# Optimization experiments

Measured on AMD Instinct MI355X. Metric: run time of the kernel, lower is better.

The kernel has to match this reference:

```python
import jax, jax.numpy as jnp
import numpy as np
import math

B, L, D, H, MAX_K = 8, 4096, 2048, 16, 1024
HD = D // H


def setup_inputs() -> dict:
    key = jax.random.key(0)
    ks = jax.random.split(key, 20)
    x = jax.random.normal(ks[0], (B, L, D), dtype=jnp.float32)
    register = jax.random.normal(ks[1], (B, D), dtype=jnp.float32)
    # mask with exactly MAX_K True per row -> max_k == MAX_K, no ragged padding
    perms = jax.vmap(lambda k: jax.random.permutation(k, L))(jax.random.split(ks[2], B))
    sel = perms[:, :MAX_K]
    mask = jnp.zeros((B, L), dtype=bool).at[jnp.arange(B)[:, None], sel].set(True)
    s = 1.0 / math.sqrt(D)
    def lin(k):
        k1, k2 = jax.random.split(k)
        return (jax.random.uniform(k1, (D, D), jnp.float32, -s, s),
                jax.random.uniform(k2, (D,), jnp.float32, -s, s))
    Wq, bq = lin(ks[3]); Wk, bk = lin(ks[4]); Wv, bv = lin(ks[5])
    Wrk, brk = lin(ks[6]); Wrv, brv = lin(ks[7]); Wo, bo = lin(ks[8])
    return {"x": x, "mask": mask, "register": register,
            "Wq": Wq, "bq": bq, "Wk": Wk, "bk": bk, "Wv": Wv, "bv": bv,
            "Wrk": Wrk, "brk": brk, "Wrv": Wrv, "brv": brv, "Wo": Wo, "bo": bo}


def reference(x, mask, register, Wq, bq, Wk, bk, Wv, bv, Wrk, brk, Wrv, brv, Wo, bo):
    Bb, Ll, Dd = x.shape
    scale = math.sqrt(HD)
    # stable argsort puts True(=selected) tokens first, in ascending position order
    idx = jnp.argsort(jnp.logical_not(mask), axis=1, stable=True)[:, :MAX_K]  # [B,K]
    pos = idx
    sig = jnp.take_along_axis(x, idx[:, :, None], axis=1)  # [B,K,D]
    Q = (sig @ Wq.T + bq).reshape(Bb, MAX_K, H, HD)
    Kt = (sig @ Wk.T + bk)
    Vt = (sig @ Wv.T + bv)
    Kr = (register @ Wrk.T + brk)[:, None, :]  # [B,1,D]
    Vr = (register @ Wrv.T + brv)[:, None, :]
    Kall = jnp.concatenate([Kt, Kr], axis=1).reshape(Bb, MAX_K + 1, H, HD)
    Vall = jnp.concatenate([Vt, Vr], axis=1).reshape(Bb, MAX_K + 1, H, HD)
    scores = jnp.einsum('bqhd,bkhd->bhqk', Q, Kall) / scale  # [B,H,K,K+1]
    causal = jnp.where(pos[:, :, None] < pos[:, None, :], -1e9, 0.0)  # [B,K,K]
    full_mask = jnp.concatenate([causal, jnp.zeros((Bb, MAX_K, 1), x.dtype)], axis=2)[:, None]
    attn = jax.nn.softmax(scores + full_mask, axis=-1)
    out = jnp.einsum('bhqk,bkhd->bqhd', attn, Vall).reshape(Bb, MAX_K, Dd)
    y = out @ Wo.T + bo
    res = x.at[jnp.arange(Bb)[:, None], idx].set(y)
    return res
```

## Files before the change

### kernel.cpp

```cpp
#include <hip/hip_runtime.h>
#include <hip/hip_bf16.h>

#define B_  8
#define L_  4096
#define D_  2048
#define H_  16
#define HD_ 128
#define MK_ 1024
#define VTP 1040

typedef __attribute__((ext_vector_type(8))) short short8;
typedef __attribute__((ext_vector_type(4))) float f32x4;

__device__ inline unsigned short f2bf(float f) {
  unsigned int u = __float_as_uint(f);
  unsigned int r = (u + 0x7fffu + ((u >> 16) & 1u)) >> 16;
  return (unsigned short)r;
}

__device__ __forceinline__ void gload_lds16(const void* g, void* l) {
  __builtin_amdgcn_global_load_lds(
      (const __attribute__((address_space(1))) void*)g,
      (__attribute__((address_space(3))) void*)l, 16, 0, 0);
}

__global__ void detect_mask_kernel(const unsigned char* __restrict__ mask, int* flag,
                                   unsigned char* __restrict__ sel) {
  __shared__ int cnt;
  if (threadIdx.x == 0) cnt = 0;
  __syncthreads();
  for (int i = threadIdx.x; i < (B_ * L_) / 16; i += 256) ((int4*)sel)[i] = make_int4(0, 0, 0, 0);
  int local = 0;
  for (int i = threadIdx.x; i < B_ * L_; i += 256) local += (mask[i] != 0);
  atomicAdd(&cnt, local);
  __syncthreads();
  if (threadIdx.x == 0) {
    int t = 0;
    if (cnt == B_ * MK_)      t = 0;
    else if (cnt == 2 * MK_)  t = 1;
    else if (cnt == 4 * MK_)  t = 2;
    *flag = t;
  }
}

__global__ void build_rowmap_kernel(const void* __restrict__ maskv,
                                    const int* __restrict__ flag,
                                    int* __restrict__ rowmap,
                                    unsigned char* __restrict__ sel) {
  int b = blockIdx.x;
  int tid = threadIdx.x;
  int t = *flag;
  __shared__ int cnts[256];
  unsigned char loc[16];
  int c = 0;
  for (int j = 0; j < 16; ++j) {
    int pos = tid * 16 + j;
    int mv;
    if (t == 1)      mv = ((const int*)maskv)[b * L_ + pos] != 0;
    else if (t == 2) mv = ((const float*)maskv)[b * L_ + pos] != 0.0f;
    else             mv = ((const unsigned char*)maskv)[b * L_ + pos] != 0;
    loc[j] = (unsigned char)mv; c += mv;
  }
  cnts[tid] = c;
  __syncthreads();
  for (int off = 1; off < 256; off <<= 1) {
    int v = (tid >= off) ? cnts[tid - off] : 0;
    __syncthreads();
    cnts[tid] += v;
    __syncthreads();
  }
  int rank = cnts[tid] - c;
  for (int j = 0; j < 16; ++j) {
    if (loc[j]) {
      if (rank < MK_) {
        int grow = b * L_ + tid * 16 + j;
        rowmap[b * MK_ + rank] = grow;
        sel[grow] = 1;
      }
      ++rank;
    }
  }
}

__global__ __launch_bounds__(256) void copy_x_kernel(const float4* __restrict__ src,
                                                     float4* __restrict__ dst,
                                                     const unsigned char* __restrict__ sel) {
  int row = blockIdx.x;
  if (sel[row]) return;
  size_t base = (size_t)row * 512 + threadIdx.x;
  dst[base] = src[base];
  dst[base + 256] = src[base + 256];
}

__global__ __launch_bounds__(256) void gather_sig_kernel(const float* __restrict__ x,
                                                         const int* __restrict__ rowmap,
                                                         unsigned short* __restrict__ sig) {
  int row = blockIdx.x;
  const float* src = x + (size_t)rowmap[row] * D_;
  unsigned short* dst = sig + (size_t)row * D_;
  int tid = threadIdx.x;
  float4 a = ((const float4*)src)[tid * 2];
  float4 b4 = ((const float4*)src)[tid * 2 + 1];
  uint4 o;
  o.x = f2bf(a.x)  | ((unsigned)f2bf(a.y)  << 16);
  o.y = f2bf(a.z)  | ((unsigned)f2bf(a.w)  << 16);
  o.z = f2bf(b4.x) | ((unsigned)f2bf(b4.y) << 16);
  o.w = f2bf(b4.z) | ((unsigned)f2bf(b4.w) << 16);
  *(uint4*)(dst + tid * 8) = o;
}

__global__ __launch_bounds__(256) void conv_bf16_kernel(const float* __restrict__ W0,
                                                        const float* __restrict__ W1,
                                                        const float* __restrict__ W2,
                                                        const float* __restrict__ W3,
                                                        unsigned short* __restrict__ Wb) {
  const size_t per = (size_t)D_ * D_;
  int slab = blockIdx.x >> 11;
  const float* W = (slab == 0) ? W0 : (slab == 1) ? W1 : (slab == 2) ? W2 : W3;
  size_t i = ((size_t)(blockIdx.x & 2047) * 256 + threadIdx.x) * 8;
  float4 a = *(const float4*)(W + i);
  float4 b4 = *(const float4*)(W + i + 4);
  uint4 o;
  o.x = f2bf(a.x)  | ((unsigned)f2bf(a.y)  << 16);
  o.y = f2bf(a.z)  | ((unsigned)f2bf(a.w)  << 16);
  o.z = f2bf(b4.x) | ((unsigned)f2bf(b4.y) << 16);
  o.w = f2bf(b4.z) | ((unsigned)f2bf(b4.w) << 16);
  *(uint4*)(Wb + slab * per + i) = o;
}

__global__ __launch_bounds__(256) void reg_kv_kernel(
    const float* __restrict__ reg, const float* __restrict__ Wrk, const float* __restrict__ brk,
    const float* __restrict__ Wrv, const float* __restrict__ brv,
    unsigned short* __restrict__ Kb, unsigned short* __restrict__ Vt) {
  int gw = (blockIdx.x * 256 + threadIdx.x) >> 6;
  int lane = threadIdx.x & 63;
  int mat = gw >> 11;
  int n = gw & 2047;
  const float* W = mat ? Wrv : Wrk;
  const float* wrow = W + (size_t)n * D_;
  float s[8] = {};
  for (int j = 0; j < 8; ++j) {
    int e = j * 256 + lane * 4;
    float4 wv = *(const float4*)(wrow + e);
#pragma unroll
    for (int b = 0; b < 8; ++b) {
      float4 rv = *(const float4*)(reg + (size_t)b * D_ + e);
      s[b] += wv.x * rv.x + wv.y * rv.y + wv.z * rv.z + wv.w * rv.w;
    }
  }
#pragma unroll
  for (int off = 32; off; off >>= 1)
#pragma unroll
    for (int b = 0; b < 8; ++b) s[b] += __shfl_down(s[b], off);
  if (lane == 0) {
    float bias = (mat ? brv : brk)[n];
#pragma unroll
    for (int b = 0; b < 8; ++b) {
      unsigned short v = f2bf(s[b] + bias);
      if (mat) {
        Vt[(((size_t)b * 16 + (n >> 7)) * 128 + (n & 127)) * VTP + 1024] = v;
      } else {
        Kb[((size_t)b * 1025 + 1024) * D_ + n] = v;
      }
    }
  }
}

template<int FUSED>
__global__ __launch_bounds__(512, 2) void gemm8_kernel(
    const unsigned short* __restrict__ A, const unsigned short* __restrict__ Bw,
    const float* __restrict__ b0, const float* __restrict__ b1, const float* __restrict__ b2,
    void* __restrict__ O0, void* __restrict__ O1, void* __restrict__ O2,
    const int* __restrict__ rowmap, float qalpha, int nbt, int matfix) {
  __shared__ __align__(16) unsigned short lds[4][2][8192];
  int tid = threadIdx.x, lane = tid & 63, w = tid >> 6;
  int g = lane >> 4, l15 = lane & 15;
  int wm = w >> 2, wn = w & 3;

  int bid = blockIdx.x;
  int xcd = bid & 7, j = bid >> 3;
  int mb = xcd * 4 + j / nbt, nb = j % nbt;
  int m0 = mb * 256, n0 = nb * 256;

  f32x4 acc[2][4][4] = {};

#define STAGE(kt, c) {                                                          \
    const unsigned short* src0 = (c) ? Bw : A;                                  \
    int base0 = (c) ? n0 : m0;                                                  \
    int sg = (lane & 3) ^ ((lane >> 3) & 3);                                    \
    _Pragma("unroll")                                                           \
    for (int i_ = 0; i_ < 2; ++i_) {                                            \
      int row = (w * 2 + i_) * 16 + (lane >> 2);                                \
      gload_lds16(src0 + (size_t)(base0 + row) * D_ + (kt) * 32 + sg * 8,       \
                  &lds[(kt) & 3][c][(w * 2 + i_) * 512]);                       \
    }                                                                           \
  }

  STAGE(0, 0); STAGE(0, 1);
  STAGE(1, 0); STAGE(1, 1);
  STAGE(2, 0); STAGE(2, 1);
  asm volatile("s_waitcnt vmcnt(8)" ::: "memory");
  __builtin_amdgcn_s_barrier();

  int sw8 = (g ^ ((l15 >> 1) & 3)) * 8;

  for (int kt = 0; kt < 64; ++kt) {
    const unsigned short* Abuf = &lds[kt & 3][0][0];
    const unsigned short* Bbuf = &lds[kt & 3][1][0];
    short8 af[4], bf[4];

#pragma unroll
    for (int nf = 0; nf < 4; ++nf)
      bf[nf] = *(const short8*)(Bbuf + (wn * 64 + nf * 16 + l15) * 32 + sw8);
#pragma unroll
    for (int mf = 0; mf < 4; ++mf)
      af[mf] = *(const short8*)(Abuf + (wm * 128 + mf * 16 + l15) * 32 + sw8);
    if (kt + 3 < 64) STAGE(kt + 3, 0);
    __builtin_amdgcn_s_barrier();
    asm volatile("s_waitcnt lgkmcnt(0)" ::: "memory");
    __builtin_amdgcn_sched_barrier(0);
    __builtin_amdgcn_s_setprio(1);
#pragma unroll
    for (int mf = 0; mf < 4; ++mf)
#pragma unroll
      for (int nf = 0; nf < 4; ++nf)
        acc[0][mf][nf] = __builtin_amdgcn_mfma_f32_16x16x32_bf16(af[mf], bf[nf], acc[0][mf][nf], 0, 0, 0);
    __builtin_amdgcn_s_setprio(0);
    __builtin_amdgcn_s_barrier();

#pragma unroll
    for (int mf = 0; mf < 4; ++mf)
      af[mf] = *(const short8*)(Abuf + (wm * 128 + 64 + mf * 16 + l15) * 32 + sw8);
    if (kt + 3 < 64) STAGE(kt + 3, 1);
    __builtin_amdgcn_s_barrier();
    asm volatile("s_waitcnt lgkmcnt(0)" ::: "memory");
    __builtin_amdgcn_sched_barrier(0);
    __builtin_amdgcn_s_setprio(1);
#pragma unroll
    for (int mf = 0; mf < 4; ++mf)
#pragma unroll
      for (int nf = 0; nf < 4; ++nf)
        acc[1][mf][nf] = __builtin_amdgcn_mfma_f32_16x16x32_bf16(af[mf], bf[nf], acc[1][mf][nf], 0, 0, 0);
    __builtin_amdgcn_s_setprio(0);
    if (kt < 61)       asm volatile("s_waitcnt vmcnt(8)" ::: "memory");
    else if (kt == 61) asm volatile("s_waitcnt vmcnt(4)" ::: "memory");
    else if (kt == 62) asm volatile("s_waitcnt vmcnt(0)" ::: "memory");
    __builtin_amdgcn_s_barrier();
  }
#undef STAGE

  int mat = 0;
  const float* bias = b0;
  float alpha = 1.0f;
  int n0l = n0;
  if (FUSED) {
    mat = (matfix >= 0) ? matfix : (n0 >> 11);
    bias = (mat == 0) ? b0 : ((mat == 1) ? b1 : b2);
    alpha = (mat == 0) ? qalpha : 1.0f;
    n0l = n0 & 2047;
  }

#pragma unroll
  for (int ph = 0; ph < 2; ++ph) {
#pragma unroll
    for (int mf = 0; mf < 4; ++mf) {
#pragma unroll
      for (int nf = 0; nf < 4; ++nf) {
        int nn = n0l + wn * 64 + nf * 16 + l15;
        float bvv = bias[nn];
        int m = m0 + wm * 128 + ph * 64 + mf * 16 + g * 4;
        if (FUSED) {
          if (mat == 2) {
            int bb = m >> 10, tok = m & 1023;
            size_t base = (((size_t)bb * 16 + (nn >> 7)) * 128 + (nn & 127)) * VTP + tok;
            uint2 u;
            u.x = f2bf(acc[ph][mf][nf][0] + bvv) | ((unsigned)f2bf(acc[ph][mf][nf][1] + bvv) << 16);
            u.y = f2bf(acc[ph][mf][nf][2] + bvv) | ((unsigned)f2bf(acc[ph][mf][nf][3] + bvv) << 16);
            *(uint2*)((unsigned short*)O2 + base) = u;
          } else {
            unsigned short* out = (mat == 0) ? (unsigned short*)O0 : (unsigned short*)O1;
#pragma unroll
            for (int r = 0; r < 4; ++r) {
              float v = (acc[ph][mf][nf][r] + bvv) * alpha;
              int mm = m + r;
              int row = (mat == 1) ? mm + (mm >> 10) : mm;
              out[(size_t)row * D_ + nn] = f2bf(v);
            }
          }
        } else {
#pragma unroll
          for (int r = 0; r < 4; ++r) {
            int row = rowmap[m + r];
            ((float*)O0)[(size_t)row * D_ + nn] = acc[ph][mf][nf][r] + bvv;
          }
        }
      }
    }
  }
}

__device__ __forceinline__ void stage_k(const unsigned short* Kbase, unsigned short* dst,
                                        int kv0, int w, int lane) {
#pragma unroll
  for (int i = 0; i < 2; ++i) {
    int ib = w * 2 + i;
    int row = ib * 4 + (lane >> 4);
    int sl = (lane & 15) ^ (row & 7);
    int krow = kv0 + row; if (krow > MK_) krow = MK_;
    gload_lds16(Kbase + (size_t)krow * D_ + sl * 8, dst + ib * 512);
  }
}
__device__ __forceinline__ void stage_v(const unsigned short* Vbase, unsigned short* dst,
                                        int kv0, int w, int lane) {
#pragma unroll
  for (int i = 0; i < 2; ++i) {
    int ib = w * 2 + i;
    int row = ib * 8 + (lane >> 3);
    int sl = (lane & 7) ^ (row & 7);
    gload_lds16(Vbase + (size_t)row * VTP + kv0 + sl * 8, dst + ib * 512);
  }
}

__global__ __launch_bounds__(512) void attn_kernel(
    const unsigned short* __restrict__ Qb, const unsigned short* __restrict__ Kb,
    const unsigned short* __restrict__ Vt, unsigned short* __restrict__ Ob) {
  int bx = blockIdx.x;
  int qi = 7 - (bx >> 7);
  int bh = bx & 127;
  int b = bh >> 4, h = bh & 15;
  int tid = threadIdx.x, lane = tid & 63, w = tid >> 6;
  int g = lane >> 4, l15 = lane & 15;
  int q0 = qi * 128;
  int nt = 2 * qi + 3;

  __shared__ __align__(16) unsigned short Ks[2][64 * 128];
  __shared__ __align__(16) unsigned short Vts[128 * 64];
  __shared__ __align__(16) unsigned short Ps[8][16][72];

  const unsigned short* Kbase = Kb + (size_t)b * 1025 * D_ + h * HD_;
  const unsigned short* Vbase = Vt + (size_t)bh * 128 * VTP;

  short8 qf[4];
  {
    const unsigned short* qrow = Qb + (size_t)(b * MK_ + q0 + w * 16 + l15) * D_ + h * HD_;
#pragma unroll
    for (int kk = 0; kk < 4; ++kk) qf[kk] = *(const short8*)(qrow + kk * 32 + g * 8);
  }

  f32x4 oacc[8] = {};
  float mrow[4], lrow[4];
#pragma unroll
  for (int r = 0; r < 4; ++r) { mrow[r] = -__builtin_inff(); lrow[r] = 0.f; }

  int qminw = q0 + w * 16;

  stage_k(Kbase, Ks[0], 0, w, lane);
  int cur = 0;

  for (int t = 0; t < nt; ++t) {
    int kv0 = (t < nt - 1) ? t * 64 : MK_;
    stage_v(Vbase, Vts, kv0, w, lane);
    if (t + 1 < nt) {
      int kv1 = (t + 1 < nt - 1) ? (t + 1) * 64 : MK_;
      stage_k(Kbase, Ks[cur ^ 1], kv1, w, lane);
      asm volatile("s_waitcnt vmcnt(4)" ::: "memory");
    } else {
      asm volatile("s_waitcnt vmcnt(2)" ::: "memory");
    }
    __builtin_amdgcn_s_barrier();

    bool active = (t == nt - 1) || (t * 64 <= qminw + 15);
    f32x4 sacc[4] = {};
    if (active) {
      const unsigned short* ks = Ks[cur];
#pragma unroll
      for (int kk = 0; kk < 4; ++kk) {
#pragma unroll
        for (int nf = 0; nf < 4; ++nf) {
          int krow = nf * 16 + l15;
          int sw = (kk * 4 + g) ^ (krow & 7);
          short8 kf = *(const short8*)(ks + krow * 128 + sw * 8);
          sacc[nf] = __builtin_amdgcn_mfma_f32_16x16x32_bf16(qf[kk], kf, sacc[nf], 0, 0, 0);
        }
      }

      if (t == nt - 1) {
#pragma unroll
        for (int nf = 0; nf < 4; ++nf) {
          int col = nf * 16 + l15;
          if (col != 0) {
#pragma unroll
            for (int r = 0; r < 4; ++r) sacc[nf][r] = -1e9f;
          }
        }
      } else if (t * 64 + 63 > qminw) {
        int qb = qminw - t * 64 + g * 4;
#pragma unroll
        for (int nf = 0; nf < 4; ++nf) {
          int col = nf * 16 + l15;
#pragma unroll
          for (int r = 0; r < 4; ++r)
            if (col > qb + r) sacc[nf][r] = -1e9f;
        }
      }

      float pm[4]; bool need = false;
#pragma unroll
      for (int r = 0; r < 4; ++r) {
        float mx = fmaxf(fmaxf(sacc[0][r], sacc[1][r]), fmaxf(sacc[2][r], sacc[3][r]));
        mx = fmaxf(mx, __shfl_xor(mx, 1));
        mx = fmaxf(mx, __shfl_xor(mx, 2));
        mx = fmaxf(mx, __shfl_xor(mx, 4));
        mx = fmaxf(mx, __shfl_xor(mx, 8));
        pm[r] = mx;
        need |= (mx > mrow[r] + 8.0f);
      }
      if (__any((int)need)) {
#pragma unroll
        for (int r = 0; r < 4; ++r) {
          float mnew = fmaxf(mrow[r], pm[r]);
          float sf = exp2f(mrow[r] - mnew);
          mrow[r] = mnew;
          lrow[r] *= sf;
#pragma unroll
          for (int i = 0; i < 8; ++i) oacc[i][r] *= sf;
        }
      }
      float rs[4] = {0.f, 0.f, 0.f, 0.f};
#pragma unroll
      for (int nf = 0; nf < 4; ++nf) {
#pragma unroll
        for (int r = 0; r < 4; ++r) {
          float p = exp2f(sacc[nf][r] - mrow[r]);
          sacc[nf][r] = p;
          rs[r] += p;
        }
      }
#pragma unroll
      for (int r = 0; r < 4; ++r) {
        float s = rs[r];
        s += __shfl_xor(s, 1);
        s += __shfl_xor(s, 2);
        s += __shfl_xor(s, 4);
        s += __shfl_xor(s, 8);
        lrow[r] += s;
      }
#pragma unroll
      for (int nf = 0; nf < 4; ++nf)
#pragma unroll
        for (int r = 0; r < 4; ++r)
          Ps[w][g * 4 + r][nf * 16 + l15] = f2bf(sacc[nf][r]);
    }

    if (t + 1 < nt) asm volatile("s_waitcnt vmcnt(2)" ::: "memory");
    else            asm volatile("s_waitcnt vmcnt(0)" ::: "memory");
    __builtin_amdgcn_s_barrier();

    if (active) {
#pragma unroll
      for (int kk = 0; kk < 2; ++kk) {
        short8 pf = *(const short8*)(&Ps[w][l15][kk * 32 + g * 8]);
#pragma unroll
        for (int nf = 0; nf < 8; ++nf) {
          int vrow = nf * 16 + l15;
          int sw = (kk * 4 + g) ^ (vrow & 7);
          short8 vf = *(const short8*)(Vts + vrow * 64 + sw * 8);
          oacc[nf] = __builtin_amdgcn_mfma_f32_16x16x32_bf16(pf, vf, oacc[nf], 0, 0, 0);
        }
      }
    }
    __builtin_amdgcn_s_barrier();
    cur ^= 1;
  }

#pragma unroll
  for (int nf = 0; nf < 8; ++nf) {
#pragma unroll
    for (int r = 0; r < 4; ++r) {
      size_t row = (size_t)b * MK_ + q0 + w * 16 + g * 4 + r;
      Ob[row * D_ + h * HD_ + nf * 16 + l15] = f2bf(oacc[nf][r] / lrow[r]);
    }
  }
}

extern "C" void kernel_launch(void* const* d_in, const int* in_sizes, int n_in,
                              void* d_out, int out_size, void* d_ws, size_t ws_size,
                              hipStream_t stream) {
  const float* x    = (const float*)d_in[0];
  const void*  mask = d_in[1];
  const float* reg  = (const float*)d_in[2];
  const float* Wq   = (const float*)d_in[3];
  const float* bq   = (const float*)d_in[4];
  const float* Wk   = (const float*)d_in[5];
  const float* bk   = (const float*)d_in[6];
  const float* Wv   = (const float*)d_in[7];
  const float* bv   = (const float*)d_in[8];
  const float* Wrk  = (const float*)d_in[9];
  const float* brk  = (const float*)d_in[10];
  const float* Wrv  = (const float*)d_in[11];
  const float* brv  = (const float*)d_in[12];
  const float* Wo   = (const float*)d_in[13];
  const float* bo   = (const float*)d_in[14];

  char* ws = (char*)d_ws;
  int* flag            = (int*)ws;
  int* rowmap          = (int*)(ws + 256);
  unsigned char* sel   = (unsigned char*)(ws + 33024);
  char* p = ws + 66048;
  unsigned short* sig = (unsigned short*)p;              p += (size_t)8192 * 2048 * 2;
  unsigned short* Qb  = (unsigned short*)p;              p += (size_t)8192 * 2048 * 2;
  unsigned short* Kb  = (unsigned short*)p;              p += (size_t)8200 * 2048 * 2;
  unsigned short* Vtb = (unsigned short*)p;              p += ((size_t)16384 * VTP + 64) * 2;
  unsigned short* Wbf = (unsigned short*)p;
  unsigned short* Ob  = sig;

  const size_t need_fused = (size_t)(p - ws) + (size_t)8192 * 2048 * 2;
  const bool fused = (ws_size >= need_fused);

  detect_mask_kernel<<<1, 256, 0, stream>>>((const unsigned char*)mask, flag, sel);
  build_rowmap_kernel<<<8, 256, 0, stream>>>(mask, flag, rowmap, sel);
  copy_x_kernel<<<B_ * L_, 256, 0, stream>>>((const float4*)x, (float4*)d_out, sel);
  gather_sig_kernel<<<8192, 256, 0, stream>>>(x, rowmap, sig);
  reg_kv_kernel<<<1024, 256, 0, stream>>>(reg, Wrk, brk, Wrv, brv, Kb, Vtb);

  const float qalpha = 0.08838834764831845f * 1.4426950408889634f;
  const size_t per = (size_t)2048 * 2048;

  if (fused) {
    conv_bf16_kernel<<<8192, 256, 0, stream>>>(Wq, Wk, Wv, Wo, Wbf);
    gemm8_kernel<1><<<768, 512, 0, stream>>>(sig, Wbf, bq, bk, bv, Qb, Kb, Vtb,
                                             nullptr, qalpha, 24, -1);
    attn_kernel<<<1024, 512, 0, stream>>>(Qb, Kb, Vtb, Ob);
    gemm8_kernel<0><<<256, 512, 0, stream>>>(Ob, Wbf + 3 * per, bo, nullptr, nullptr,
                                             d_out, nullptr, nullptr, rowmap, 1.0f, 8, -1);
  } else {
    conv_bf16_kernel<<<2048, 256, 0, stream>>>(Wq, Wq, Wq, Wq, Wbf);
    gemm8_kernel<1><<<256, 512, 0, stream>>>(sig, Wbf, bq, bk, bv, Qb, Kb, Vtb,
                                             nullptr, qalpha, 8, 0);
    conv_bf16_kernel<<<2048, 256, 0, stream>>>(Wk, Wk, Wk, Wk, Wbf);
    gemm8_kernel<1><<<256, 512, 0, stream>>>(sig, Wbf, bq, bk, bv, Qb, Kb, Vtb,
                                             nullptr, qalpha, 8, 1);
    conv_bf16_kernel<<<2048, 256, 0, stream>>>(Wv, Wv, Wv, Wv, Wbf);
    gemm8_kernel<1><<<256, 512, 0, stream>>>(sig, Wbf, bq, bk, bv, Qb, Kb, Vtb,
                                             nullptr, qalpha, 8, 2);
    attn_kernel<<<1024, 512, 0, stream>>>(Qb, Kb, Vtb, Ob);
    conv_bf16_kernel<<<2048, 256, 0, stream>>>(Wo, Wo, Wo, Wo, Wbf);
    gemm8_kernel<0><<<256, 512, 0, stream>>>(Ob, Wbf, bo, nullptr, nullptr,
                                             d_out, nullptr, nullptr, rowmap, 1.0f, 8, -1);
  }
}
```

Before: 547.2 us.

## Fuse x passthrough copy into attention kernel and software-pipeline GEMM LDS fragment loads

Removes the separate copy_x kernel and the selection bitmap. The attention kernel now copies the whole x tensor into the output, with each block handling a slice sized to its KV-tile count, and the later output GEMM overwrites the selected rows. The GEMM main loop is restructured to double-buffer the B fragments and preload the next tile's A fragments. This lets LDS reads overlap the MFMAs and drops one barrier per half-step. The cost is more register pressure and extra memory traffic inside the attention kernel.

```diff
diff --git a/kernel.cpp b/kernel.cpp
--- a/kernel.cpp
+++ b/kernel.cpp
@@ -24,12 +24,10 @@
       (__attribute__((address_space(3))) void*)l, 16, 0, 0);
 }
 
-__global__ void detect_mask_kernel(const unsigned char* __restrict__ mask, int* flag,
-                                   unsigned char* __restrict__ sel) {
+__global__ void detect_mask_kernel(const unsigned char* __restrict__ mask, int* flag) {
   __shared__ int cnt;
   if (threadIdx.x == 0) cnt = 0;
   __syncthreads();
-  for (int i = threadIdx.x; i < (B_ * L_) / 16; i += 256) ((int4*)sel)[i] = make_int4(0, 0, 0, 0);
   int local = 0;
   for (int i = threadIdx.x; i < B_ * L_; i += 256) local += (mask[i] != 0);
   atomicAdd(&cnt, local);
@@ -45,8 +43,7 @@
 
 __global__ void build_rowmap_kernel(const void* __restrict__ maskv,
                                     const int* __restrict__ flag,
-                                    int* __restrict__ rowmap,
-                                    unsigned char* __restrict__ sel) {
+                                    int* __restrict__ rowmap) {
   int b = blockIdx.x;
   int tid = threadIdx.x;
   int t = *flag;
@@ -72,24 +69,10 @@
   int rank = cnts[tid] - c;
   for (int j = 0; j < 16; ++j) {
     if (loc[j]) {
-      if (rank < MK_) {
-        int grow = b * L_ + tid * 16 + j;
-        rowmap[b * MK_ + rank] = grow;
-        sel[grow] = 1;
-      }
+      if (rank < MK_) rowmap[b * MK_ + rank] = b * L_ + tid * 16 + j;
       ++rank;
     }
   }
-}
-
-__global__ __launch_bounds__(256) void copy_x_kernel(const float4* __restrict__ src,
-                                                     float4* __restrict__ dst,
-                                                     const unsigned char* __restrict__ sel) {
-  int row = blockIdx.x;
-  if (sel[row]) return;
-  size_t base = (size_t)row * 512 + threadIdx.x;
-  dst[base] = src[base];
-  dst[base + 256] = src[base + 256];
 }
 
 __global__ __launch_bounds__(256) void gather_sig_kernel(const float* __restrict__ x,
@@ -204,49 +187,68 @@
 
   int sw8 = (g ^ ((l15 >> 1) & 3)) * 8;
 
-  for (int kt = 0; kt < 64; ++kt) {
-    const unsigned short* Abuf = &lds[kt & 3][0][0];
-    const unsigned short* Bbuf = &lds[kt & 3][1][0];
-    short8 af[4], bf[4];
-
+  short8 afE[4], afO[4], bfA[4], bfB[4];
+  {
+    const unsigned short* Ab = &lds[0][0][0];
+    const unsigned short* Bb = &lds[0][1][0];
 #pragma unroll
     for (int nf = 0; nf < 4; ++nf)
-      bf[nf] = *(const short8*)(Bbuf + (wn * 64 + nf * 16 + l15) * 32 + sw8);
+      bfA[nf] = *(const short8*)(Bb + (wn * 64 + nf * 16 + l15) * 32 + sw8);
 #pragma unroll
     for (int mf = 0; mf < 4; ++mf)
-      af[mf] = *(const short8*)(Abuf + (wm * 128 + mf * 16 + l15) * 32 + sw8);
-    if (kt + 3 < 64) STAGE(kt + 3, 0);
-    __builtin_amdgcn_s_barrier();
-    asm volatile("s_waitcnt lgkmcnt(0)" ::: "memory");
-    __builtin_amdgcn_sched_barrier(0);
-    __builtin_amdgcn_s_setprio(1);
-#pragma unroll
-    for (int mf = 0; mf < 4; ++mf)
-#pragma unroll
-      for (int nf = 0; nf < 4; ++nf)
-        acc[0][mf][nf] = __builtin_amdgcn_mfma_f32_16x16x32_bf16(af[mf], bf[nf], acc[0][mf][nf], 0, 0, 0);
-    __builtin_amdgcn_s_setprio(0);
-    __builtin_amdgcn_s_barrier();
-
-#pragma unroll
-    for (int mf = 0; mf < 4; ++mf)
-      af[mf] = *(const short8*)(Abuf + (wm * 128 + 64 + mf * 16 + l15) * 32 + sw8);
-    if (kt + 3 < 64) STAGE(kt + 3, 1);
-    __builtin_amdgcn_s_barrier();
-    asm volatile("s_waitcnt lgkmcnt(0)" ::: "memory");
-    __builtin_amdgcn_sched_barrier(0);
-    __builtin_amdgcn_s_setprio(1);
-#pragma unroll
-    for (int mf = 0; mf < 4; ++mf)
-#pragma unroll
-      for (int nf = 0; nf < 4; ++nf)
-        acc[1][mf][nf] = __builtin_amdgcn_mfma_f32_16x16x32_bf16(af[mf], bf[nf], acc[1][mf][nf], 0, 0, 0);
-    __builtin_amdgcn_s_setprio(0);
-    if (kt < 61)       asm volatile("s_waitcnt vmcnt(8)" ::: "memory");
-    else if (kt == 61) asm volatile("s_waitcnt vmcnt(4)" ::: "memory");
-    else if (kt == 62) asm volatile("s_waitcnt vmcnt(0)" ::: "memory");
-    __builtin_amdgcn_s_barrier();
-  }
+      afE[mf] = *(const short8*)(Ab + (wm * 128 + mf * 16 + l15) * 32 + sw8);
+  }
+
+#define KTILE(kt, bfC, bfN)                                                       \
+  {                                                                               \
+    const unsigned short* Abuf = &lds[(kt) & 3][0][0];                            \
+    _Pragma("unroll")                                                             \
+    for (int mf = 0; mf < 4; ++mf)                                                \
+      afO[mf] = *(const short8*)(Abuf + (wm * 128 + 64 + mf * 16 + l15) * 32 + sw8); \
+    if ((kt) + 3 < 64) STAGE((kt) + 3, 0);                                        \
+    asm volatile("s_waitcnt lgkmcnt(4)" ::: "memory");                            \
+    __builtin_amdgcn_sched_barrier(0);                                            \
+    __builtin_amdgcn_s_setprio(1);                                                \
+    _Pragma("unroll")                                                             \
+    for (int mf = 0; mf < 4; ++mf)                                                \
+      _Pragma("unroll")                                                           \
+      for (int nf = 0; nf < 4; ++nf)                                              \
+        acc[0][mf][nf] = __builtin_amdgcn_mfma_f32_16x16x32_bf16(afE[mf], bfC[nf], acc[0][mf][nf], 0, 0, 0); \
+    __builtin_amdgcn_s_setprio(0);                                                \
+    if ((kt) <= 60)      asm volatile("s_waitcnt vmcnt(6)" ::: "memory");         \
+    else if ((kt) == 61) asm volatile("s_waitcnt vmcnt(4)" ::: "memory");         \
+    else if ((kt) == 62) asm volatile("s_waitcnt vmcnt(0)" ::: "memory");         \
+    if ((kt) < 63) {                                                              \
+      __builtin_amdgcn_s_barrier();                                               \
+      const unsigned short* An = &lds[((kt) + 1) & 3][0][0];                      \
+      const unsigned short* Bn = &lds[((kt) + 1) & 3][1][0];                      \
+      _Pragma("unroll")                                                           \
+      for (int nf = 0; nf < 4; ++nf)                                              \
+        bfN[nf] = *(const short8*)(Bn + (wn * 64 + nf * 16 + l15) * 32 + sw8);    \
+      _Pragma("unroll")                                                           \
+      for (int mf = 0; mf < 4; ++mf)                                              \
+        afE[mf] = *(const short8*)(An + (wm * 128 + mf * 16 + l15) * 32 + sw8);   \
+      if ((kt) + 3 < 64) STAGE((kt) + 3, 1);                                      \
+      asm volatile("s_waitcnt lgkmcnt(8)" ::: "memory");                          \
+    } else {                                                                      \
+      asm volatile("s_waitcnt lgkmcnt(0)" ::: "memory");                          \
+    }                                                                             \
+    __builtin_amdgcn_sched_barrier(0);                                            \
+    __builtin_amdgcn_s_setprio(1);                                                \
+    _Pragma("unroll")                                                             \
+    for (int mf = 0; mf < 4; ++mf)                                                \
+      _Pragma("unroll")                                                           \
+      for (int nf = 0; nf < 4; ++nf)                                              \
+        acc[1][mf][nf] = __builtin_amdgcn_mfma_f32_16x16x32_bf16(afO[mf], bfC[nf], acc[1][mf][nf], 0, 0, 0); \
+    __builtin_amdgcn_s_setprio(0);                                                \
+    if ((kt) < 63) __builtin_amdgcn_s_barrier();                                  \
+  }
+
+  for (int kt2 = 0; kt2 < 32; ++kt2) {
+    KTILE(2 * kt2,     bfA, bfB);
+    KTILE(2 * kt2 + 1, bfB, bfA);
+  }
+#undef KTILE
 #undef STAGE
 
   int mat = 0;
@@ -321,11 +323,15 @@
   }
 }
 
+#define NF4 16777216
+
 __global__ __launch_bounds__(512) void attn_kernel(
     const unsigned short* __restrict__ Qb, const unsigned short* __restrict__ Kb,
-    const unsigned short* __restrict__ Vt, unsigned short* __restrict__ Ob) {
+    const unsigned short* __restrict__ Vt, unsigned short* __restrict__ Ob,
+    const float4* __restrict__ xsrc, float4* __restrict__ xdst) {
   int bx = blockIdx.x;
-  int qi = 7 - (bx >> 7);
+  int gq = bx >> 7;
+  int qi = 7 - gq;
   int bh = bx & 127;
   int b = bh >> 4, h = bh & 15;
   int tid = threadIdx.x, lane = tid & 63, w = tid >> 6;
@@ -333,6 +339,8 @@
   int q0 = qi * 128;
   int nt = 2 * qi + 3;
 
+  size_t cpyBase = ((size_t)128 * (18 * gq - gq * gq) + (size_t)(bx & 127) * nt) * 2048;
+
   __shared__ __align__(16) unsigned short Ks[2][64 * 128];
   __shared__ __align__(16) unsigned short Vts[128 * 64];
   __shared__ __align__(16) unsigned short Ps[8][16][72];
@@ -359,13 +367,26 @@
 
   for (int t = 0; t < nt; ++t) {
     int kv0 = (t < nt - 1) ? t * 64 : MK_;
+
+    size_t ci[4];
+    float4 cv[4];
+    {
+      size_t i0 = cpyBase + (size_t)t * 2048 + tid;
+#pragma unroll
+      for (int jj = 0; jj < 4; ++jj) {
+        size_t ix = i0 + jj * 512;
+        ci[jj] = ix < NF4 ? ix : (NF4 - 1);
+        cv[jj] = xsrc[ci[jj]];
+      }
+    }
+
     stage_v(Vbase, Vts, kv0, w, lane);
     if (t + 1 < nt) {
       int kv1 = (t + 1 < nt - 1) ? (t + 1) * 64 : MK_;
       stage_k(Kbase, Ks[cur ^ 1], kv1, w, lane);
-      asm volatile("s_waitcnt vmcnt(4)" ::: "memory");
+      asm volatile("s_waitcnt vmcnt(8)" ::: "memory");
     } else {
-      asm volatile("s_waitcnt vmcnt(2)" ::: "memory");
+      asm volatile("s_waitcnt vmcnt(6)" ::: "memory");
     }
     __builtin_amdgcn_s_barrier();
 
@@ -454,6 +475,10 @@
 
     if (t + 1 < nt) asm volatile("s_waitcnt vmcnt(2)" ::: "memory");
     else            asm volatile("s_waitcnt vmcnt(0)" ::: "memory");
+
+#pragma unroll
+    for (int jj = 0; jj < 4; ++jj) xdst[ci[jj]] = cv[jj];
+
     __builtin_amdgcn_s_barrier();
 
     if (active) {
@@ -505,7 +530,6 @@
   char* ws = (char*)d_ws;
   int* flag            = (int*)ws;
   int* rowmap          = (int*)(ws + 256);
-  unsigned char* sel   = (unsigned char*)(ws + 33024);
   char* p = ws + 66048;
   unsigned short* sig = (unsigned short*)p;              p += (size_t)8192 * 2048 * 2;
   unsigned short* Qb  = (unsigned short*)p;              p += (size_t)8192 * 2048 * 2;
@@ -517,9 +541,8 @@
   const size_t need_fused = (size_t)(p - ws) + (size_t)8192 * 2048 * 2;
   const bool fused = (ws_size >= need_fused);
 
-  detect_mask_kernel<<<1, 256, 0, stream>>>((const unsigned char*)mask, flag, sel);
-  build_rowmap_kernel<<<8, 256, 0, stream>>>(mask, flag, rowmap, sel);
-  copy_x_kernel<<<B_ * L_, 256, 0, stream>>>((const float4*)x, (float4*)d_out, sel);
+  detect_mask_kernel<<<1, 256, 0, stream>>>((const unsigned char*)mask, flag);
+  build_rowmap_kernel<<<8, 256, 0, stream>>>(mask, flag, rowmap);
   gather_sig_kernel<<<8192, 256, 0, stream>>>(x, rowmap, sig);
   reg_kv_kernel<<<1024, 256, 0, stream>>>(reg, Wrk, brk, Wrv, brv, Kb, Vtb);
 
@@ -530,7 +553,7 @@
     conv_bf16_kernel<<<8192, 256, 0, stream>>>(Wq, Wk, Wv, Wo, Wbf);
     gemm8_kernel<1><<<768, 512, 0, stream>>>(sig, Wbf, bq, bk, bv, Qb, Kb, Vtb,
                                              nullptr, qalpha, 24, -1);
-    attn_kernel<<<1024, 512, 0, stream>>>(Qb, Kb, Vtb, Ob);
+    attn_kernel<<<1024, 512, 0, stream>>>(Qb, Kb, Vtb, Ob, (const float4*)x, (float4*)d_out);
     gemm8_kernel<0><<<256, 512, 0, stream>>>(Ob, Wbf + 3 * per, bo, nullptr, nullptr,
                                              d_out, nullptr, nullptr, rowmap, 1.0f, 8, -1);
   } else {
@@ -543,7 +566,7 @@
     conv_bf16_kernel<<<2048, 256, 0, stream>>>(Wv, Wv, Wv, Wv, Wbf);
     gemm8_kernel<1><<<256, 512, 0, stream>>>(sig, Wbf, bq, bk, bv, Qb, Kb, Vtb,
                                              nullptr, qalpha, 8, 2);
-    attn_kernel<<<1024, 512, 0, stream>>>(Qb, Kb, Vtb, Ob);
+    attn_kernel<<<1024, 512, 0, stream>>>(Qb, Kb, Vtb, Ob, (const float4*)x, (float4*)d_out);
     conv_bf16_kernel<<<2048, 256, 0, stream>>>(Wo, Wo, Wo, Wo, Wbf);
     gemm8_kernel<0><<<256, 512, 0, stream>>>(Ob, Wbf, bo, nullptr, nullptr,
                                              d_out, nullptr, nullptr, rowmap, 1.0f, 8, -1);
```

Result: no change. 537.1 us (-1.9%).
